# Kernel tuning notes

Measured on AMD Instinct MI355X. Metric: run time of the kernel, lower is better.

The kernel has to match this reference:

```python
import jax, jax.numpy as jnp
import numpy as np

N = 10000      # nodes
E = 320000     # edges (avg degree 32)
H = 128        # hidden_channels
G = 50         # num_gaussians
NF = 128       # num_filters
L = 6          # num_interactions
CUTOFF = 10.0


def ssp(x):
    # ShiftedSoftplus: softplus(x) - log(2)
    return jax.nn.softplus(x) - jnp.log(2.0).astype(x.dtype)


def setup_inputs() -> dict:
    key = jax.random.key(0)
    ks = jax.random.split(key, 16)
    s = 0.05
    return {
        "z": jax.random.normal(ks[0], (N, H), jnp.float32),
        "pos": jax.random.normal(ks[1], (N, 3), jnp.float32) * 3.0,
        "edge_index": jax.random.randint(ks[2], (2, E), 0, N, dtype=jnp.int64),
        # per-layer stacked parameters (PyTorch Linear convention: y = x @ W.T + b)
        "mlp1_w": jax.random.normal(ks[3], (L, NF, G), jnp.float32) * s,
        "mlp1_b": jnp.zeros((L, NF), jnp.float32),
        "mlp2_w": jax.random.normal(ks[4], (L, NF, NF), jnp.float32) * s,
        "mlp2_b": jnp.zeros((L, NF), jnp.float32),
        "lin1_w": jax.random.normal(ks[5], (L, NF, H), jnp.float32) * s,   # no bias
        "lin2_w": jax.random.normal(ks[6], (L, H, NF), jnp.float32) * s,
        "lin2_b": jnp.zeros((L, H), jnp.float32),
        "lin_w": jax.random.normal(ks[7], (L, H, H), jnp.float32) * s,
        "lin_b": jnp.zeros((L, H), jnp.float32),
        "coord_w": jax.random.normal(ks[8], (L, 1, G + 2 * H), jnp.float32) * s,
        "coord_b": jnp.zeros((L, 1), jnp.float32),
    }


def reference(z, pos, edge_index, mlp1_w, mlp1_b, mlp2_w, mlp2_b,
              lin1_w, lin2_w, lin2_b, lin_w, lin_b, coord_w, coord_b):
    row, col = edge_index[0], edge_index[1]
    # edge distances from INITIAL positions (computed once, as in torch code)
    edge_weight = jnp.linalg.norm(pos[row] - pos[col], axis=-1)          # [E]
    offset = jnp.linspace(0.0, CUTOFF, G).astype(pos.dtype)              # [G]
    coeff = -0.5 / (offset[1] - offset[0]) ** 2
    edge_attr = jnp.exp(coeff * (edge_weight[:, None] - offset[None, :]) ** 2)  # [E,G]
    C = 0.5 * (jnp.cos(edge_weight * jnp.pi / CUTOFF) + 1.0)             # [E] cosine cutoff
    ones_e = jnp.ones((E,), pos.dtype)
    h = z
    for l in range(L):
        # ---- coordinate update (uses current pos and current h) ----
        feat = jnp.concatenate([edge_attr, h[row], h[col]], axis=-1)     # [E, G+2H]
        cw = feat @ coord_w[l].T + coord_b[l]                            # [E,1]
        aggr = (pos[row] - pos[col]) * cw                                # [E,3]
        sums = jax.ops.segment_sum(aggr, row, num_segments=N)            # [N,3]
        cnt = jax.ops.segment_sum(ones_e, row, num_segments=N)           # [N]
        mean = jnp.where(cnt[:, None] > 0, sums / jnp.maximum(cnt, 1.0)[:, None], 0.0)
        pos = pos + mean
        # ---- CFConv interaction ----
        Wf = ssp(edge_attr @ mlp1_w[l].T + mlp1_b[l]) @ mlp2_w[l].T + mlp2_b[l]  # [E,NF]
        Wf = Wf * C[:, None]
        xf = h @ lin1_w[l].T                                             # [N,NF]
        agg = jax.ops.segment_sum(xf[row] * Wf, col, num_segments=N)     # [N,NF]
        out = agg @ lin2_w[l].T + lin2_b[l]                              # [N,H]
        h = h + (ssp(out) @ lin_w[l].T + lin_b[l])
    return (pos, h)
```

## Files before the change

### kernel.cpp

```cpp
#include <hip/hip_runtime.h>


#define NN 10000
#define EE 320000
#define HH 128
#define GG 50
#define NF 128
#define NL 6
#define TROWS 2048
#define NB 128

typedef unsigned short u16;
typedef unsigned int u32;
typedef short bf16x8 __attribute__((ext_vector_type(8)));
typedef float f32x4  __attribute__((ext_vector_type(4)));

__device__ __forceinline__ float us2f(u16 u){
  union { float f; u32 i; } v; v.i = ((u32)u) << 16; return v.f;
}
__device__ __forceinline__ u16 f2us(float x){
  union { float f; u32 i; } v; v.f = x;
  u32 r = v.i + 0x7fffu + ((v.i >> 16) & 1u);
  return (u16)(r >> 16);
}
__device__ __forceinline__ float ldin(const void* p, int i, int bf){
  return bf ? us2f(((const u16*)p)[i]) : ((const float*)p)[i];
}
__device__ __forceinline__ float sspf(float x){
  return fmaxf(x, 0.f) + __logf(1.f + __expf(-fabsf(x))) - 0.6931472f;
}
__device__ __forceinline__ int detect_bf(const u32* __restrict__ zraw){
  int lane = threadIdx.x & 63;
  int c = 0;
  #pragma unroll
  for(int j=0;j<4;j++){
    u32 w = zraw[lane*4+j];
    u32 hb = (w >> 8) & 0x7F;
    c += (hb >= 0x38 && hb <= 0x41) ? 1 : 0;
  }
  return __popcll(__ballot(c >= 2)) >= 32;
}
__device__ __forceinline__ int detect_i64(const int* __restrict__ ei_raw){
  int lane = threadIdx.x & 63;
  int c = 0;
  #pragma unroll
  for(int j=0;j<4;j++) c += (ei_raw[2*(lane*4+j)+1] == 0) ? 1 : 0;
  return __popcll(__ballot(c >= 3)) >= 32;
}

__global__ void k_prep(const u32* __restrict__ zraw, const void* __restrict__ pos_in,
    const void* __restrict__ mlp1_w, const void* __restrict__ mlp1_b,
    const void* __restrict__ mlp2_w, const void* __restrict__ mlp2_b,
    const void* __restrict__ lin1_w, const void* __restrict__ lin2_w,
    const void* __restrict__ lin2_b, const void* __restrict__ lin_w,
    const void* __restrict__ lin_b,  const void* __restrict__ coord_w,
    const void* __restrict__ coord_b,
    float* __restrict__ h, float* __restrict__ pc40, int* __restrict__ wmaxi,
    float* __restrict__ b1f, float* __restrict__ b2v,
    u16* __restrict__ w1b, u16* __restrict__ w2bb,
    u16* __restrict__ l1b, u16* __restrict__ l2b,
    float* __restrict__ l2bf, u16* __restrict__ lwb,
    float* __restrict__ lbf, float* __restrict__ cwf, float* __restrict__ cbf)
{
  int bf = detect_bf(zraw);
  int b = blockIdx.x;
  if(b < NN*HH/256){
    int i = b*256 + threadIdx.x;
    h[i] = ldin(zraw, i, bf);
    if(i < NN*3){
      int n = i/3, comp = i%3;
      pc40[n*4 + comp] = ldin(pos_in, i, bf);
    }
    if(i == 0) *wmaxi = 0;
  } else {
    int i = (b - NN*HH/256)*256 + threadIdx.x;
    if(i < NL*NF){
      b1f[i]  = ldin(mlp1_b, i, bf);
      b2v[i]  = ldin(mlp2_b, i, bf);
      l2bf[i] = ldin(lin2_b, i, bf);
      lbf[i]  = ldin(lin_b,  i, bf);
    }
    if(i < NL*NF*64){
      int l = i/(NF*64), rem = i%(NF*64);
      int f = rem>>6, g = rem&63;
      w1b[i] = (g < GG) ? f2us(ldin(mlp1_w, (l*NF + f)*GG + g, bf)) : (u16)0;
    }
    if(i < NL*NF*NF){
      w2bb[i] = f2us(ldin(mlp2_w, i, bf));
      l1b[i]  = f2us(ldin(lin1_w, i, bf));
      l2b[i]  = f2us(ldin(lin2_w, i, bf));
      lwb[i]  = f2us(ldin(lin_w,  i, bf));
    }
    if(i < NL*(GG+2*HH)) cwf[i] = ldin(coord_w, i, bf);
    if(i < NL) cbf[i] = ldin(coord_b, i, bf);
  }
}

__global__ void k_count(const int* __restrict__ ei_raw, const float* __restrict__ pc4,
                        int* __restrict__ eiN, float* __restrict__ wE,
                        u32* __restrict__ partR32, u32* __restrict__ partC32,
                        int* __restrict__ wmaxi){
  __shared__ u32 hr[NN/2];
  __shared__ u32 hc[NN/2];
  int is64 = detect_i64(ei_raw);
  int b = blockIdx.x, tid = threadIdx.x;
  for(int i=tid; i<NN/2; i+=256){ hr[i]=0; hc[i]=0; }
  __syncthreads();
  int e0 = b*(EE/NB), e1 = e0 + EE/NB;
  float wm = 0.f;
  for(int e = e0 + tid; e < e1; e += 256){
    int r = is64 ? ei_raw[2*e] : ei_raw[e];
    int c = is64 ? ei_raw[2*(EE+e)] : ei_raw[EE+e];
    eiN[e] = r; eiN[EE+e] = c;
    float4 pr = *(const float4*)&pc4[r*4];
    float4 pcv = *(const float4*)&pc4[c*4];
    float dx = pr.x-pcv.x, dy = pr.y-pcv.y, dz = pr.z-pcv.z;
    float w = sqrtf(dx*dx + dy*dy + dz*dz);
    wE[e] = w;
    wm = fmaxf(wm, w);
    atomicAdd(&hr[r>>1], (r&1) ? 0x10000u : 1u);
    atomicAdd(&hc[c>>1], (c&1) ? 0x10000u : 1u);
  }
  #pragma unroll
  for(int s=32; s>0; s>>=1) wm = fmaxf(wm, __shfl_down(wm, s, 64));
  if((tid & 63) == 0) atomicMax(wmaxi, __float_as_int(wm));
  __syncthreads();
  for(int i=tid; i<NN/2; i+=256){
    partR32[(size_t)b*(NN/2) + i] = hr[i];
    partC32[(size_t)b*(NN/2) + i] = hc[i];
  }
}

__global__ void k_scan2(const int* __restrict__ col_deg, const int* __restrict__ deg_row,
                        int* __restrict__ col_start, int* __restrict__ row_start){
  __shared__ int pc[1024];
  __shared__ int pr[1024];
  int tid = threadIdx.x;
  const int CH = (NN + 1023)/1024;
  int base = tid*CH;
  int sc = 0, sr = 0;
  for(int i=0;i<CH;i++){
    int idx = base+i;
    if(idx<NN){ sc += col_deg[idx]; sr += deg_row[idx]; }
  }
  pc[tid] = sc; pr[tid] = sr;
  __syncthreads();
  for(int off=1; off<1024; off<<=1){
    int vc = (tid>=off) ? pc[tid-off] : 0;
    int vr = (tid>=off) ? pr[tid-off] : 0;
    __syncthreads();
    pc[tid] += vc; pr[tid] += vr;
    __syncthreads();
  }
  int runc = (tid==0) ? 0 : pc[tid-1];
  int runr = (tid==0) ? 0 : pr[tid-1];
  for(int i=0;i<CH;i++){
    int idx = base+i;
    if(idx<NN){
      col_start[idx]=runc; runc += col_deg[idx];
      row_start[idx]=runr; runr += deg_row[idx];
    }
  }
  if(tid==1023){ col_start[NN] = runc; row_start[NN] = runr; }
}

__global__ void k_fill(const int* __restrict__ eiN, const float* __restrict__ wE,
                       const int* __restrict__ col_start, const int* __restrict__ row_start,
                       const u16* __restrict__ partR16, const u16* __restrict__ partC16,
                       int* __restrict__ row_s, float* __restrict__ wEs,
                       int* __restrict__ rcol_s, float* __restrict__ rw_s){
  __shared__ u32 hr[NN/2];
  __shared__ u32 hc[NN/2];
  int b = blockIdx.x, t = threadIdx.x;
  for(int i=t; i<NN/2; i+=256){ hr[i]=0; hc[i]=0; }
  __syncthreads();
  int e0 = b*(EE/NB), e1 = e0 + EE/NB;
  for(int e = e0 + t; e < e1; e += 256){
    int r = eiN[e], c = eiN[EE+e];
    float w = wE[e];
    u32 oldc = atomicAdd(&hc[c>>1], (c&1) ? 0x10000u : 1u);
    u32 rkc = (c&1) ? (oldc >> 16) : (oldc & 0xFFFFu);
    int p = col_start[c] + (int)partC16[(size_t)b*NN + c] + (int)rkc;
    row_s[p] = r; wEs[p] = w;
    u32 oldr = atomicAdd(&hr[r>>1], (r&1) ? 0x10000u : 1u);
    u32 rkr = (r&1) ? (oldr >> 16) : (oldr & 0xFFFFu);
    int p2 = row_start[r] + (int)partR16[(size_t)b*NN + r] + (int)rkr;
    rcol_s[p2] = c; rw_s[p2] = w;
  }
}

__global__ void k_tabnode(const u16* __restrict__ w1b, const float* __restrict__ b1f,
                          const u16* __restrict__ w2bb, const float* __restrict__ b2v,
                          const float* __restrict__ cwf, const int* __restrict__ wmaxi,
                          u16* __restrict__ tabB, float* __restrict__ tabS,
                          const float* __restrict__ h, const u16* __restrict__ l1b,
                          u16* __restrict__ xfb0, float* __restrict__ dr0,
                          float* __restrict__ pc40,
                          u16* __restrict__ partR16, u16* __restrict__ partC16,
                          int* __restrict__ degR, int* __restrict__ degC){
  __shared__ __align__(16) u16 S[32*72 + 32*136];
  int b = blockIdx.x, t = threadIdx.x;
  int wave = t >> 6, lane = t & 63;
  int m16 = lane & 15, quad = lane >> 4;
  if(b < NL*64){
    int l = b >> 6;
    int r0 = (b & 63)*32;
    u16* attr = S;
    u16* t1   = S + 32*72;
    float delta = __int_as_float(*wmaxi) / (float)(TROWS-1);
    for(int idx=t; idx<32*64; idx+=256){
      int r = idx >> 6, g = idx & 63;
      float w = (float)(r0 + r)*delta;
      float d = w - (float)g*(10.f/49.f);
      attr[r*72 + g] = (g < GG) ? f2us(__expf(-12.005f*d*d)) : (u16)0;
    }
    __syncthreads();
    {
      const u16* __restrict__ w1 = w1b + (size_t)l*NF*64;
      f32x4 acc[2][2];
      #pragma unroll
      for(int nc=0;nc<2;nc++){
        float bv = b1f[l*NF + wave*32 + nc*16 + m16];
        #pragma unroll
        for(int mr=0;mr<2;mr++) acc[mr][nc] = (f32x4){bv,bv,bv,bv};
      }
      #pragma unroll
      for(int ks=0; ks<2; ks++){
        bf16x8 aA[2], bB[2];
        #pragma unroll
        for(int mr=0;mr<2;mr++)
          aA[mr] = *(const bf16x8*)&attr[(mr*16 + m16)*72 + ks*32 + quad*8];
        #pragma unroll
        for(int nc=0;nc<2;nc++)
          bB[nc] = *(const bf16x8*)&w1[(wave*32 + nc*16 + m16)*64 + ks*32 + quad*8];
        #pragma unroll
        for(int mr=0;mr<2;mr++)
          #pragma unroll
          for(int nc=0;nc<2;nc++)
            acc[mr][nc] = __builtin_amdgcn_mfma_f32_16x16x32_bf16(aA[mr], bB[nc], acc[mr][nc], 0,0,0);
      }
      #pragma unroll
      for(int mr=0;mr<2;mr++)
        #pragma unroll
        for(int nc=0;nc<2;nc++)
          #pragma unroll
          for(int r=0;r<4;r++)
            t1[(mr*16 + quad*4 + r)*136 + wave*32 + nc*16 + m16] = f2us(sspf(acc[mr][nc][r]));
    }
    __syncthreads();
    {
      const u16* __restrict__ w2 = w2bb + (size_t)l*NF*NF;
      f32x4 acc[2][2];
      #pragma unroll
      for(int nc=0;nc<2;nc++){
        float bv = b2v[l*NF + wave*32 + nc*16 + m16];
        #pragma unroll
        for(int mr=0;mr<2;mr++) acc[mr][nc] = (f32x4){bv,bv,bv,bv};
      }
      #pragma unroll
      for(int ks=0; ks<4; ks++){
        bf16x8 aA[2], bB[2];
        #pragma unroll
        for(int mr=0;mr<2;mr++)
          aA[mr] = *(const bf16x8*)&t1[(mr*16 + m16)*136 + ks*32 + quad*8];
        #pragma unroll
        for(int nc=0;nc<2;nc++)
          bB[nc] = *(const bf16x8*)&w2[(wave*32 + nc*16 + m16)*NF + ks*32 + quad*8];
        #pragma unroll
        for(int mr=0;mr<2;mr++)
          #pragma unroll
          for(int nc=0;nc<2;nc++)
            acc[mr][nc] = __builtin_amdgcn_mfma_f32_16x16x32_bf16(aA[mr], bB[nc], acc[mr][nc], 0,0,0);
      }
      #pragma unroll
      for(int mr=0;mr<2;mr++){
        #pragma unroll
        for(int r=0;r<4;r++){
          int row = r0 + mr*16 + quad*4 + r;
          float w = (float)row*delta;
          float C = 0.5f*(cosf(w*0.3141592653589793f) + 1.f);
          #pragma unroll
          for(int nc=0;nc<2;nc++)
            tabB[((size_t)l*TROWS + row)*NF + wave*32 + nc*16 + m16] = f2us(acc[mr][nc][r]*C);
        }
      }
    }
    if(t < 32){
      const float* __restrict__ cwg = cwf + l*(GG+2*HH);
      float w = (float)(r0 + t)*delta;
      float s = 0.f;
      for(int g=0; g<GG; g++){
        float d = w - (float)g*(10.f/49.f);
        s += __expf(-12.005f*d*d)*cwg[g];
      }
      tabS[l*TROWS + r0 + t] = s;
    }
  } else if(b < NL*64 + NN/16){
    int n0 = (b - NL*64)*16;
    u16* T = S;
    {
      int node = t >> 4, c0 = (t & 15)*8;
      const float* hp = &h[(n0 + node)*HH + c0];
      f32x4 v0 = *(const f32x4*)hp;
      f32x4 v1 = *(const f32x4*)(hp+4);
      u16* d = &T[node*136 + c0];
      d[0]=f2us(v0[0]); d[1]=f2us(v0[1]); d[2]=f2us(v0[2]); d[3]=f2us(v0[3]);
      d[4]=f2us(v1[0]); d[5]=f2us(v1[1]); d[6]=f2us(v1[2]); d[7]=f2us(v1[3]);
    }
    __syncthreads();
    {
      const float* __restrict__ cw = cwf;
      int j = t >> 4, l16 = t & 15;
      float ar = 0.f, ac = 0.f;
      #pragma unroll
      for(int i=0;i<8;i++){
        float hvv = us2f(T[j*136 + l16 + 16*i]);
        ar += hvv*cw[GG + l16 + 16*i];
        ac += hvv*cw[GG + HH + l16 + 16*i];
      }
      #pragma unroll
      for(int s=8; s>0; s>>=1){
        ar += __shfl_down(ar, s, 16);
        ac += __shfl_down(ac, s, 16);
      }
      if(l16 == 0){ dr0[n0+j] = ar; pc40[(n0+j)*4+3] = ac; }
    }
    {
      const u16* __restrict__ wC = l1b;
      bf16x8 aH[4];
      #pragma unroll
      for(int ks=0; ks<4; ks++)
        aH[ks] = *(const bf16x8*)&T[m16*136 + ks*32 + quad*8];
      #pragma unroll
      for(int nc=0; nc<2; nc++){
        int fcol = wave*32 + nc*16 + m16;
        f32x4 acc = (f32x4){0.f,0.f,0.f,0.f};
        #pragma unroll
        for(int ks=0; ks<4; ks++){
          bf16x8 bbv = *(const bf16x8*)&wC[fcol*HH + ks*32 + quad*8];
          acc = __builtin_amdgcn_mfma_f32_16x16x32_bf16(aH[ks], bbv, acc, 0,0,0);
        }
        #pragma unroll
        for(int r=0;r<4;r++)
          xfb0[(n0+quad*4+r)*NF + fcol] = f2us(acc[r]);
      }
    }
  } else {
    int n = (b - (NL*64 + NN/16))*256 + t;
    if(n >= NN) return;
    u32 rr = 0, rc = 0;
    for(int b0=0; b0<NB; b0+=8){
      u32 vr[8], vc[8];
      #pragma unroll
      for(int j=0;j<8;j++){
        vr[j] = partR16[(size_t)(b0+j)*NN + n];
        vc[j] = partC16[(size_t)(b0+j)*NN + n];
      }
      #pragma unroll
      for(int j=0;j<8;j++){
        partR16[(size_t)(b0+j)*NN + n] = (u16)rr; rr += vr[j];
        partC16[(size_t)(b0+j)*NN + n] = (u16)rc; rc += vc[j];
      }
    }
    degR[n] = (int)rr; degC[n] = (int)rc;
  }
}

__global__ void k_layer(const int* __restrict__ col_start, const int* __restrict__ row_s,
                        const float* __restrict__ wEs, const u32* __restrict__ xfR,
                        u16* __restrict__ xfW,
                        const u16* __restrict__ tabB, const int* __restrict__ wmaxi,
                        int l,
                        const u16* __restrict__ l2b, const float* __restrict__ l2bf,
                        const u16* __restrict__ lwb, const float* __restrict__ lbf,
                        float* __restrict__ h, const u16* __restrict__ l1b,
                        const float* __restrict__ cwf,
                        const float* __restrict__ drR, float* __restrict__ drW,
                        const int* __restrict__ row_start, const int* __restrict__ rcol_s,
                        const float* __restrict__ rw_s, const float* __restrict__ tabS,
                        const float* __restrict__ cbf,
                        const float* __restrict__ pc4R, float* __restrict__ pc4W,
                        const u32* __restrict__ zraw, void* __restrict__ out){
  __shared__ __align__(16) u16 T[16*136];
  __shared__ __align__(16) u16 T2[16*136];
  int b = blockIdx.x, t = threadIdx.x;
  float invD = (float)(TROWS-1) / __int_as_float(*wmaxi);
  int wave = t >> 6, lane = t & 63;

  if(b % 3 == 0){
    int n0 = (b/3)*16;
    {
      const u32* __restrict__ tg32 = (const u32*)(tabB + (size_t)l*TROWS*NF);
      u32* __restrict__ T32 = (u32*)T;
      #pragma unroll
      for(int j=0;j<2;j++){
        int n = n0 + wave*2 + j;
        int p0 = col_start[n], p1 = col_start[n+1];
        float aa[4] = {0.f,0.f,0.f,0.f};
        float bb[4] = {0.f,0.f,0.f,0.f};
        int p = p0;
        for(; p+8 <= p1; p += 8){
          u32 gv[8], xv[8];
          #pragma unroll
          for(int k=0;k<8;k++){
            int r = row_s[p+k];
            int i0 = min((int)(wEs[p+k]*invD + 0.5f), TROWS-1);
            gv[k] = tg32[i0*64 + lane];
            xv[k] = xfR[r*64 + lane];
          }
          #pragma unroll
          for(int k=0;k<8;k++){
            aa[k&3] += us2f((u16)xv[k])      * us2f((u16)gv[k]);
            bb[k&3] += us2f((u16)(xv[k]>>16))* us2f((u16)(gv[k]>>16));
          }
        }
        for(; p < p1; p++){
          int r = row_s[p];
          int i0 = min((int)(wEs[p]*invD + 0.5f), TROWS-1);
          u32 g = tg32[i0*64 + lane];
          u32 x = xfR[r*64 + lane];
          aa[0] += us2f((u16)x)      * us2f((u16)g);
          bb[0] += us2f((u16)(x>>16))* us2f((u16)(g>>16));
        }
        float av = (aa[0]+aa[1])+(aa[2]+aa[3]);
        float bv = (bb[0]+bb[1])+(bb[2]+bb[3]);
        T32[(wave*2+j)*68 + lane] = (u32)f2us(av) | ((u32)f2us(bv) << 16);
      }
    }
    __syncthreads();
    int m16 = lane & 15, quad = lane >> 4;
    int fcol = wave*16 + m16;
    f32x4 acc;
    {
      bf16x8 aA[4];
      #pragma unroll
      for(int ks=0; ks<4; ks++)
        aA[ks] = *(const bf16x8*)&T[m16*136 + ks*32 + quad*8];
      const u16* __restrict__ wA = l2b + l*HH*NF;
      float bv = l2bf[l*HH + fcol];
      acc = (f32x4){bv,bv,bv,bv};
      #pragma unroll
      for(int ks=0; ks<4; ks++){
        bf16x8 bbv = *(const bf16x8*)&wA[fcol*NF + ks*32 + quad*8];
        acc = __builtin_amdgcn_mfma_f32_16x16x32_bf16(aA[ks], bbv, acc, 0,0,0);
      }
      #pragma unroll
      for(int r=0;r<4;r++)
        T2[(quad*4+r)*136 + fcol] = f2us(sspf(acc[r]));
    }
    __syncthreads();
    float hv[4];
    int bf = (l == NL-1) ? detect_bf(zraw) : 0;
    {
      bf16x8 aS[4];
      #pragma unroll
      for(int ks=0; ks<4; ks++)
        aS[ks] = *(const bf16x8*)&T2[m16*136 + ks*32 + quad*8];
      const u16* __restrict__ wB = lwb + l*HH*HH;
      float bv = lbf[l*HH + fcol];
      acc = (f32x4){bv,bv,bv,bv};
      #pragma unroll
      for(int ks=0; ks<4; ks++){
        bf16x8 bbv = *(const bf16x8*)&wB[fcol*HH + ks*32 + quad*8];
        acc = __builtin_amdgcn_mfma_f32_16x16x32_bf16(aS[ks], bbv, acc, 0,0,0);
      }
      #pragma unroll
      for(int r=0;r<4;r++)
        hv[r] = h[(n0+quad*4+r)*HH + fcol] + acc[r];
    }
    if(l == NL-1){
      #pragma unroll
      for(int r=0;r<4;r++){
        int n = n0 + quad*4 + r;
        if(bf) ((u16*)out)[NN*3 + n*HH + fcol] = f2us(hv[r]);
        else   ((float*)out)[NN*3 + n*HH + fcol] = hv[r];
      }
      return;
    }
    #pragma unroll
    for(int r=0;r<4;r++){
      int n = n0 + quad*4 + r;
      h[n*HH + fcol] = hv[r];
      T[(quad*4+r)*136 + fcol] = f2us(hv[r]);
    }
    __syncthreads();
    {
      bf16x8 aH[4];
      #pragma unroll
      for(int ks=0; ks<4; ks++)
        aH[ks] = *(const bf16x8*)&T[m16*136 + ks*32 + quad*8];
      const u16* __restrict__ wC = l1b + (l+1)*NF*HH;
      acc = (f32x4){0.f,0.f,0.f,0.f};
      #pragma unroll
      for(int ks=0; ks<4; ks++){
        bf16x8 bbv = *(const bf16x8*)&wC[fcol*HH + ks*32 + quad*8];
        acc = __builtin_amdgcn_mfma_f32_16x16x32_bf16(aH[ks], bbv, acc, 0,0,0);
      }
      #pragma unroll
      for(int r=0;r<4;r++)
        xfW[(n0+quad*4+r)*NF + fcol] = f2us(acc[r]);
    }
    {
      const float* __restrict__ cw = cwf + (l+1)*(GG + 2*HH);
      int j = t >> 5, l32 = t & 31;
      float ar = 0.f, ac = 0.f;
      #pragma unroll
      for(int i=0;i<4;i++){
        float hvv = us2f(T[j*136 + l32 + 32*i]);
        ar += hvv*cw[GG + l32 + 32*i];
        ac += hvv*cw[GG + HH + l32 + 32*i];
      }
      #pragma unroll
      for(int s=16; s>0; s>>=1){
        ar += __shfl_down(ar, s, 32);
        ac += __shfl_down(ac, s, 32);
      }
      if(l32 == 0){ drW[n0+j] = ar; pc4W[(n0+j)*4+3] = ac; }
    }
  } else {
    int u = b - b/3 - 1;
    int bf = (l == NL-1) ? detect_bf(zraw) : 0;
    int n = u*8 + wave;
    const float* __restrict__ ts = tabS + l*TROWS;
    float cb = cbf[l] + drR[n];
    int p0 = row_start[n], p1 = row_start[n+1];
    float4 pn = *(const float4*)&pc4R[n*4];
    float sx=0.f, sy=0.f, sz=0.f;
    for(int p = p0 + lane; p < p1; p += 64){
      int c = rcol_s[p];
      int i0 = min((int)(rw_s[p]*invD + 0.5f), TROWS-1);
      float4 pcv = *(const float4*)&pc4R[c*4];
      float a = cb + pcv.w + ts[i0];
      sx += (pn.x - pcv.x)*a;
      sy += (pn.y - pcv.y)*a;
      sz += (pn.z - pcv.z)*a;
    }
    #pragma unroll
    for(int s=32; s>0; s>>=1){
      sx += __shfl_down(sx, s, 64);
      sy += __shfl_down(sy, s, 64);
      sz += __shfl_down(sz, s, 64);
    }
    if(lane == 0){
      int cnt = p1 - p0;
      float inv = (cnt > 0) ? 1.f/(float)cnt : 0.f;
      float ox = pn.x + sx*inv, oy = pn.y + sy*inv, oz = pn.z + sz*inv;
      if(l == NL-1){
        if(bf){
          u16* o = (u16*)out;
          o[n*3+0] = f2us(ox); o[n*3+1] = f2us(oy); o[n*3+2] = f2us(oz);
        } else {
          float* o = (float*)out;
          o[n*3+0] = ox; o[n*3+1] = oy; o[n*3+2] = oz;
        }
      } else {
        pc4W[n*4+0] = ox; pc4W[n*4+1] = oy; pc4W[n*4+2] = oz;
      }
    }
  }
}

extern "C" void kernel_launch(void* const* d_in, const int* in_sizes, int n_in,
                              void* d_out, int out_size, void* d_ws, size_t ws_size,
                              hipStream_t stream){
  const u32*  z      = (const u32*)d_in[0];
  const void* pos_in = d_in[1];
  const int*  ei_raw = (const int*)d_in[2];
  const void* mlp1_w = d_in[3];
  const void* mlp1_b = d_in[4];
  const void* mlp2_w = d_in[5];
  const void* mlp2_b = d_in[6];
  const void* lin1_w = d_in[7];
  const void* lin2_w = d_in[8];
  const void* lin2_b = d_in[9];
  const void* lin_w  = d_in[10];
  const void* lin_b  = d_in[11];
  const void* coord_w= d_in[12];
  const void* coord_b= d_in[13];

  float* W = (float*)d_ws;
  float* h    = W; W += NN*HH;
  float* pc40 = W; W += NN*4;
  float* pc41 = W; W += NN*4;
  float* dr0  = W; W += NN;
  float* dr1  = W; W += NN;
  float* wE   = W; W += EE;
  float* wEs  = W; W += EE;
  float* rw_s = W; W += EE;
  float* b1f  = W; W += NL*NF;
  float* b2v  = W; W += NL*NF;
  float* l2bf = W; W += NL*HH;
  float* lbf  = W; W += NL*HH;
  float* cwf  = W; W += NL*(GG+2*HH);
  float* cbf  = W; W += NL;
  W = (float*)(((uintptr_t)W + 63) & ~(uintptr_t)63);
  u16*  tabB = (u16*)W; W += (size_t)NL*TROWS*NF/2;
  float* tabS = W; W += NL*TROWS;
  u16* w1b  = (u16*)W; W += (NL*NF*64)/2;
  u16* w2bb = (u16*)W; W += (NL*NF*NF)/2;
  u16* l1b  = (u16*)W; W += (NL*NF*NF)/2;
  u16* l2b  = (u16*)W; W += (NL*NF*NF)/2;
  u16* lwb  = (u16*)W; W += (NL*NF*NF)/2;
  u16* xfb0 = (u16*)W; W += (NN*NF)/2;
  u16* xfb1 = (u16*)W; W += (NN*NF)/2;
  u16* partR16 = (u16*)W; W += (size_t)NB*NN/2;
  u16* partC16 = (u16*)W; W += (size_t)NB*NN/2;
  int* degR      = (int*)W; W += NN;
  int* degC      = (int*)W; W += NN;
  int* col_start = (int*)W; W += NN+1;
  int* row_start = (int*)W; W += NN+1;
  int* row_s     = (int*)W; W += EE;
  int* rcol_s    = (int*)W; W += EE;
  int* eiN       = (int*)W; W += 2*EE;
  int* wmaxi     = (int*)W; W += 1;

  k_prep<<<NN*HH/256 + NL*NF*NF/256, 256, 0, stream>>>(
      z, pos_in, mlp1_w, mlp1_b, mlp2_w, mlp2_b, lin1_w, lin2_w, lin2_b,
      lin_w, lin_b, coord_w, coord_b,
      h, pc40, wmaxi,
      b1f, b2v, w1b, w2bb, l1b, l2b, l2bf, lwb, lbf, cwf, cbf);
  k_count<<<NB, 256, 0, stream>>>(ei_raw, pc40, eiN, wE,
                                  (u32*)partR16, (u32*)partC16, wmaxi);
  k_tabnode<<<NL*64 + NN/16 + (NN+255)/256, 256, 0, stream>>>(
      w1b, b1f, w2bb, b2v, cwf, wmaxi, tabB, tabS,
      h, l1b, xfb0, dr0, pc40,
      partR16, partC16, degR, degC);
  k_scan2<<<1, 1024, 0, stream>>>(degC, degR, col_start, row_start);
  k_fill<<<NB, 256, 0, stream>>>(eiN, wE, col_start, row_start, partR16, partC16,
                                 row_s, wEs, rcol_s, rw_s);

  for(int l=0; l<NL; l++){
    int par = l & 1;
    const u32* xfR = (const u32*)(par ? xfb1 : xfb0);
    u16* xfW = par ? xfb0 : xfb1;
    const float* drR = par ? dr1 : dr0;   float* drW = par ? dr0 : dr1;
    const float* p4R = par ? pc41 : pc40; float* p4W = par ? pc40 : pc41;
    k_layer<<<3*(NN/16), 512, 0, stream>>>(
        col_start, row_s, wEs, xfR, xfW, tabB, wmaxi, l,
        l2b, l2bf, lwb, lbf, h, l1b, cwf,
        drR, drW,
        row_start, rcol_s, rw_s, tabS, cbf, p4R, p4W, z, d_out);
  }
}
```

Measured before the change: 383.6 us.

## Record per-edge ranks in count pass, parallelize fill, double-buffer gather loads

The count kernel now saves each edge's local rank from its shared-memory atomic into per-edge u16 arrays. This lets the fill kernel become a flat one-thread-per-edge scatter over many blocks instead of 128 blocks that redo the shared histogram atomics. Separately, the per-node gather loop in the layer kernel is software-pipelined with two register buffers, so the next eight loads are issued before the current eight are consumed. The cost is extra global traffic for the rank arrays and higher register pressure in the layer kernel.

```diff
diff --git a/kernel.cpp b/kernel.cpp
--- a/kernel.cpp
+++ b/kernel.cpp
@@ -99,6 +99,7 @@
 __global__ void k_count(const int* __restrict__ ei_raw, const float* __restrict__ pc4,
                         int* __restrict__ eiN, float* __restrict__ wE,
                         u32* __restrict__ partR32, u32* __restrict__ partC32,
+                        u16* __restrict__ rkR16, u16* __restrict__ rkC16,
                         int* __restrict__ wmaxi){
   __shared__ u32 hr[NN/2];
   __shared__ u32 hc[NN/2];
@@ -118,8 +119,10 @@
     float w = sqrtf(dx*dx + dy*dy + dz*dz);
     wE[e] = w;
     wm = fmaxf(wm, w);
-    atomicAdd(&hr[r>>1], (r&1) ? 0x10000u : 1u);
-    atomicAdd(&hc[c>>1], (c&1) ? 0x10000u : 1u);
+    u32 or_ = atomicAdd(&hr[r>>1], (r&1) ? 0x10000u : 1u);
+    rkR16[e] = (u16)((r&1) ? (or_ >> 16) : (or_ & 0xFFFFu));
+    u32 oc_ = atomicAdd(&hc[c>>1], (c&1) ? 0x10000u : 1u);
+    rkC16[e] = (u16)((c&1) ? (oc_ >> 16) : (oc_ & 0xFFFFu));
   }
   #pragma unroll
   for(int s=32; s>0; s>>=1) wm = fmaxf(wm, __shfl_down(wm, s, 64));
@@ -167,26 +170,18 @@
 __global__ void k_fill(const int* __restrict__ eiN, const float* __restrict__ wE,
                        const int* __restrict__ col_start, const int* __restrict__ row_start,
                        const u16* __restrict__ partR16, const u16* __restrict__ partC16,
+                       const u16* __restrict__ rkR16, const u16* __restrict__ rkC16,
                        int* __restrict__ row_s, float* __restrict__ wEs,
                        int* __restrict__ rcol_s, float* __restrict__ rw_s){
-  __shared__ u32 hr[NN/2];
-  __shared__ u32 hc[NN/2];
-  int b = blockIdx.x, t = threadIdx.x;
-  for(int i=t; i<NN/2; i+=256){ hr[i]=0; hc[i]=0; }
-  __syncthreads();
-  int e0 = b*(EE/NB), e1 = e0 + EE/NB;
-  for(int e = e0 + t; e < e1; e += 256){
-    int r = eiN[e], c = eiN[EE+e];
-    float w = wE[e];
-    u32 oldc = atomicAdd(&hc[c>>1], (c&1) ? 0x10000u : 1u);
-    u32 rkc = (c&1) ? (oldc >> 16) : (oldc & 0xFFFFu);
-    int p = col_start[c] + (int)partC16[(size_t)b*NN + c] + (int)rkc;
-    row_s[p] = r; wEs[p] = w;
-    u32 oldr = atomicAdd(&hr[r>>1], (r&1) ? 0x10000u : 1u);
-    u32 rkr = (r&1) ? (oldr >> 16) : (oldr & 0xFFFFu);
-    int p2 = row_start[r] + (int)partR16[(size_t)b*NN + r] + (int)rkr;
-    rcol_s[p2] = c; rw_s[p2] = w;
-  }
+  int e = blockIdx.x*256 + threadIdx.x;
+  if(e >= EE) return;
+  int r = eiN[e], c = eiN[EE+e];
+  float w = wE[e];
+  int b = e / (EE/NB);
+  int p = col_start[c] + (int)partC16[(size_t)b*NN + c] + (int)rkC16[e];
+  row_s[p] = r; wEs[p] = w;
+  int p2 = row_start[r] + (int)partR16[(size_t)b*NN + r] + (int)rkR16[e];
+  rcol_s[p2] = c; rw_s[p2] = w;
 }
 
 __global__ void k_tabnode(const u16* __restrict__ w1b, const float* __restrict__ b1f,
@@ -398,22 +393,43 @@
         int p0 = col_start[n], p1 = col_start[n+1];
         float aa[4] = {0.f,0.f,0.f,0.f};
         float bb[4] = {0.f,0.f,0.f,0.f};
+        u32 gA[8], xA[8], gB[8], xB[8];
+#define LOAD8(G,X,Q) { \
+        _Pragma("unroll") \
+        for(int k=0;k<8;k++){ \
+          int r_ = row_s[(Q)+k]; \
+          int i0_ = min((int)(wEs[(Q)+k]*invD + 0.5f), TROWS-1); \
+          G[k] = tg32[i0_*64 + lane]; \
+          X[k] = xfR[r_*64 + lane]; \
+        } }
+#define CONS8(G,X) { \
+        _Pragma("unroll") \
+        for(int k=0;k<8;k++){ \
+          aa[k&3] += us2f((u16)X[k])      * us2f((u16)G[k]); \
+          bb[k&3] += us2f((u16)(X[k]>>16))* us2f((u16)(G[k]>>16)); \
+        } }
         int p = p0;
-        for(; p+8 <= p1; p += 8){
-          u32 gv[8], xv[8];
-          #pragma unroll
-          for(int k=0;k<8;k++){
-            int r = row_s[p+k];
-            int i0 = min((int)(wEs[p+k]*invD + 0.5f), TROWS-1);
-            gv[k] = tg32[i0*64 + lane];
-            xv[k] = xfR[r*64 + lane];
+        int nb = (p1 - p0) >> 3;
+        if(nb){
+          LOAD8(gA,xA,p);
+          int i = 1;
+          for(; i+1 < nb; i += 2){
+            LOAD8(gB,xB, p + i*8);
+            CONS8(gA,xA);
+            LOAD8(gA,xA, p + i*8 + 8);
+            CONS8(gB,xB);
           }
-          #pragma unroll
-          for(int k=0;k<8;k++){
-            aa[k&3] += us2f((u16)xv[k])      * us2f((u16)gv[k]);
-            bb[k&3] += us2f((u16)(xv[k]>>16))* us2f((u16)(gv[k]>>16));
+          if(i < nb){
+            LOAD8(gB,xB, p + i*8);
+            CONS8(gA,xA);
+            CONS8(gB,xB);
+          } else {
+            CONS8(gA,xA);
           }
+          p += nb*8;
         }
+#undef LOAD8
+#undef CONS8
         for(; p < p1; p++){
           int r = row_s[p];
           int i0 = min((int)(wEs[p]*invD + 0.5f), TROWS-1);
@@ -605,6 +621,8 @@
   u16* xfb1 = (u16*)W; W += (NN*NF)/2;
   u16* partR16 = (u16*)W; W += (size_t)NB*NN/2;
   u16* partC16 = (u16*)W; W += (size_t)NB*NN/2;
+  u16* rkR16 = (u16*)W; W += EE/2;
+  u16* rkC16 = (u16*)W; W += EE/2;
   int* degR      = (int*)W; W += NN;
   int* degC      = (int*)W; W += NN;
   int* col_start = (int*)W; W += NN+1;
@@ -620,14 +638,15 @@
       h, pc40, wmaxi,
       b1f, b2v, w1b, w2bb, l1b, l2b, l2bf, lwb, lbf, cwf, cbf);
   k_count<<<NB, 256, 0, stream>>>(ei_raw, pc40, eiN, wE,
-                                  (u32*)partR16, (u32*)partC16, wmaxi);
+                                  (u32*)partR16, (u32*)partC16, rkR16, rkC16, wmaxi);
   k_tabnode<<<NL*64 + NN/16 + (NN+255)/256, 256, 0, stream>>>(
       w1b, b1f, w2bb, b2v, cwf, wmaxi, tabB, tabS,
       h, l1b, xfb0, dr0, pc40,
       partR16, partC16, degR, degC);
   k_scan2<<<1, 1024, 0, stream>>>(degC, degR, col_start, row_start);
-  k_fill<<<NB, 256, 0, stream>>>(eiN, wE, col_start, row_start, partR16, partC16,
-                                 row_s, wEs, rcol_s, rw_s);
+  k_fill<<<EE/256, 256, 0, stream>>>(eiN, wE, col_start, row_start,
+                                     partR16, partC16, rkR16, rkC16,
+                                     row_s, wEs, rcol_s, rw_s);
 
   for(int l=0; l<NL; l++){
     int par = l & 1;
```

New measurement: 397.7 us. +3.7%, slower.

## Pack sorted edge source and distance bin into one word; rebalance layer blocks

Applied to the files above, without the earlier changes.

The CSR edge arrays now store a single 32-bit word per edge, holding the node index and the precomputed table bin. This replaces a separate int and float plus a per-layer quantisation step, which cuts gather traffic in every layer. The fill kernel no longer recomputes ranks with shared-memory atomics. k_count records per-edge ranks, and k_fill becomes one thread per edge. The layer kernel changes its block split from 1 conv block (16 nodes) per 2 coord blocks to 1 conv block (8 nodes, one wave each) per coord block. The MFMA tiles are now half-empty, with zero padding rows and masked stores.

```diff
diff --git a/kernel.cpp b/kernel.cpp
--- a/kernel.cpp
+++ b/kernel.cpp
@@ -99,6 +99,7 @@
 __global__ void k_count(const int* __restrict__ ei_raw, const float* __restrict__ pc4,
                         int* __restrict__ eiN, float* __restrict__ wE,
                         u32* __restrict__ partR32, u32* __restrict__ partC32,
+                        u16* __restrict__ rkR16, u16* __restrict__ rkC16,
                         int* __restrict__ wmaxi){
   __shared__ u32 hr[NN/2];
   __shared__ u32 hc[NN/2];
@@ -118,8 +119,10 @@
     float w = sqrtf(dx*dx + dy*dy + dz*dz);
     wE[e] = w;
     wm = fmaxf(wm, w);
-    atomicAdd(&hr[r>>1], (r&1) ? 0x10000u : 1u);
-    atomicAdd(&hc[c>>1], (c&1) ? 0x10000u : 1u);
+    u32 or_ = atomicAdd(&hr[r>>1], (r&1) ? 0x10000u : 1u);
+    rkR16[e] = (u16)((r&1) ? (or_ >> 16) : (or_ & 0xFFFFu));
+    u32 oc_ = atomicAdd(&hc[c>>1], (c&1) ? 0x10000u : 1u);
+    rkC16[e] = (u16)((c&1) ? (oc_ >> 16) : (oc_ & 0xFFFFu));
   }
   #pragma unroll
   for(int s=32; s>0; s>>=1) wm = fmaxf(wm, __shfl_down(wm, s, 64));
@@ -167,26 +170,19 @@
 __global__ void k_fill(const int* __restrict__ eiN, const float* __restrict__ wE,
                        const int* __restrict__ col_start, const int* __restrict__ row_start,
                        const u16* __restrict__ partR16, const u16* __restrict__ partC16,
-                       int* __restrict__ row_s, float* __restrict__ wEs,
-                       int* __restrict__ rcol_s, float* __restrict__ rw_s){
-  __shared__ u32 hr[NN/2];
-  __shared__ u32 hc[NN/2];
-  int b = blockIdx.x, t = threadIdx.x;
-  for(int i=t; i<NN/2; i+=256){ hr[i]=0; hc[i]=0; }
-  __syncthreads();
-  int e0 = b*(EE/NB), e1 = e0 + EE/NB;
-  for(int e = e0 + t; e < e1; e += 256){
-    int r = eiN[e], c = eiN[EE+e];
-    float w = wE[e];
-    u32 oldc = atomicAdd(&hc[c>>1], (c&1) ? 0x10000u : 1u);
-    u32 rkc = (c&1) ? (oldc >> 16) : (oldc & 0xFFFFu);
-    int p = col_start[c] + (int)partC16[(size_t)b*NN + c] + (int)rkc;
-    row_s[p] = r; wEs[p] = w;
-    u32 oldr = atomicAdd(&hr[r>>1], (r&1) ? 0x10000u : 1u);
-    u32 rkr = (r&1) ? (oldr >> 16) : (oldr & 0xFFFFu);
-    int p2 = row_start[r] + (int)partR16[(size_t)b*NN + r] + (int)rkr;
-    rcol_s[p2] = c; rw_s[p2] = w;
-  }
+                       const u16* __restrict__ rkR16, const u16* __restrict__ rkC16,
+                       const int* __restrict__ wmaxi,
+                       u32* __restrict__ pk_s, u32* __restrict__ pkr_s){
+  int e = blockIdx.x*256 + threadIdx.x;
+  if(e >= EE) return;
+  int r = eiN[e], c = eiN[EE+e];
+  float invD = (float)(TROWS-1) / __int_as_float(*wmaxi);
+  u32 i0 = (u32)min((int)(wE[e]*invD + 0.5f), TROWS-1);
+  int b = e / (EE/NB);
+  int p = col_start[c] + (int)partC16[(size_t)b*NN + c] + (int)rkC16[e];
+  pk_s[p] = ((u32)r << 11) | i0;
+  int p2 = row_start[r] + (int)partR16[(size_t)b*NN + r] + (int)rkR16[e];
+  pkr_s[p2] = ((u32)c << 11) | i0;
 }
 
 __global__ void k_tabnode(const u16* __restrict__ w1b, const float* __restrict__ b1f,
@@ -366,66 +362,59 @@
   }
 }
 
-__global__ void k_layer(const int* __restrict__ col_start, const int* __restrict__ row_s,
-                        const float* __restrict__ wEs, const u32* __restrict__ xfR,
-                        u16* __restrict__ xfW,
-                        const u16* __restrict__ tabB, const int* __restrict__ wmaxi,
-                        int l,
+__global__ void k_layer(const int* __restrict__ col_start, const u32* __restrict__ pk_s,
+                        const u32* __restrict__ xfR, u16* __restrict__ xfW,
+                        const u16* __restrict__ tabB, int l,
                         const u16* __restrict__ l2b, const float* __restrict__ l2bf,
                         const u16* __restrict__ lwb, const float* __restrict__ lbf,
                         float* __restrict__ h, const u16* __restrict__ l1b,
                         const float* __restrict__ cwf,
                         const float* __restrict__ drR, float* __restrict__ drW,
-                        const int* __restrict__ row_start, const int* __restrict__ rcol_s,
-                        const float* __restrict__ rw_s, const float* __restrict__ tabS,
-                        const float* __restrict__ cbf,
+                        const int* __restrict__ row_start, const u32* __restrict__ pkr_s,
+                        const float* __restrict__ tabS, const float* __restrict__ cbf,
                         const float* __restrict__ pc4R, float* __restrict__ pc4W,
                         const u32* __restrict__ zraw, void* __restrict__ out){
   __shared__ __align__(16) u16 T[16*136];
   __shared__ __align__(16) u16 T2[16*136];
   int b = blockIdx.x, t = threadIdx.x;
-  float invD = (float)(TROWS-1) / __int_as_float(*wmaxi);
   int wave = t >> 6, lane = t & 63;
 
-  if(b % 3 == 0){
-    int n0 = (b/3)*16;
+  if((b & 1) == 0){
+    int n0 = (b >> 1)*8;
     {
       const u32* __restrict__ tg32 = (const u32*)(tabB + (size_t)l*TROWS*NF);
       u32* __restrict__ T32 = (u32*)T;
-      #pragma unroll
-      for(int j=0;j<2;j++){
-        int n = n0 + wave*2 + j;
-        int p0 = col_start[n], p1 = col_start[n+1];
-        float aa[4] = {0.f,0.f,0.f,0.f};
-        float bb[4] = {0.f,0.f,0.f,0.f};
-        int p = p0;
-        for(; p+8 <= p1; p += 8){
-          u32 gv[8], xv[8];
-          #pragma unroll
-          for(int k=0;k<8;k++){
-            int r = row_s[p+k];
-            int i0 = min((int)(wEs[p+k]*invD + 0.5f), TROWS-1);
-            gv[k] = tg32[i0*64 + lane];
-            xv[k] = xfR[r*64 + lane];
-          }
-          #pragma unroll
-          for(int k=0;k<8;k++){
-            aa[k&3] += us2f((u16)xv[k])      * us2f((u16)gv[k]);
-            bb[k&3] += us2f((u16)(xv[k]>>16))* us2f((u16)(gv[k]>>16));
-          }
+      int n = n0 + wave;
+      int p0 = col_start[n], p1 = col_start[n+1];
+      float aa[4] = {0.f,0.f,0.f,0.f};
+      float bb[4] = {0.f,0.f,0.f,0.f};
+      int p = p0;
+      for(; p+8 <= p1; p += 8){
+        u32 pk[8], gv[8], xv[8];
+        #pragma unroll
+        for(int k=0;k<8;k++) pk[k] = pk_s[p+k];
+        #pragma unroll
+        for(int k=0;k<8;k++){
+          gv[k] = tg32[(pk[k] & 2047u)*64 + lane];
+          xv[k] = xfR[(pk[k] >> 11)*64 + lane];
         }
-        for(; p < p1; p++){
-          int r = row_s[p];
-          int i0 = min((int)(wEs[p]*invD + 0.5f), TROWS-1);
-          u32 g = tg32[i0*64 + lane];
-          u32 x = xfR[r*64 + lane];
-          aa[0] += us2f((u16)x)      * us2f((u16)g);
-          bb[0] += us2f((u16)(x>>16))* us2f((u16)(g>>16));
+        #pragma unroll
+        for(int k=0;k<8;k++){
+          aa[k&3] += us2f((u16)xv[k])      * us2f((u16)gv[k]);
+          bb[k&3] += us2f((u16)(xv[k]>>16))* us2f((u16)(gv[k]>>16));
         }
-        float av = (aa[0]+aa[1])+(aa[2]+aa[3]);
-        float bv = (bb[0]+bb[1])+(bb[2]+bb[3]);
-        T32[(wave*2+j)*68 + lane] = (u32)f2us(av) | ((u32)f2us(bv) << 16);
-      }
+      }
+      for(; p < p1; p++){
+        u32 pk = pk_s[p];
+        u32 g = tg32[(pk & 2047u)*64 + lane];
+        u32 x = xfR[(pk >> 11)*64 + lane];
+        aa[0] += us2f((u16)x)      * us2f((u16)g);
+        bb[0] += us2f((u16)(x>>16))* us2f((u16)(g>>16));
+      }
+      float av = (aa[0]+aa[1])+(aa[2]+aa[3]);
+      float bv = (bb[0]+bb[1])+(bb[2]+bb[3]);
+      T32[wave*68 + lane] = (u32)f2us(av) | ((u32)f2us(bv) << 16);
+      T32[(8+wave)*68 + lane] = 0;
     }
     __syncthreads();
     int m16 = lane & 15, quad = lane >> 4;
@@ -464,24 +453,30 @@
         bf16x8 bbv = *(const bf16x8*)&wB[fcol*HH + ks*32 + quad*8];
         acc = __builtin_amdgcn_mfma_f32_16x16x32_bf16(aS[ks], bbv, acc, 0,0,0);
       }
-      #pragma unroll
-      for(int r=0;r<4;r++)
-        hv[r] = h[(n0+quad*4+r)*HH + fcol] + acc[r];
+      if(quad < 2){
+        #pragma unroll
+        for(int r=0;r<4;r++)
+          hv[r] = h[(n0+quad*4+r)*HH + fcol] + acc[r];
+      }
     }
     if(l == NL-1){
+      if(quad < 2){
+        #pragma unroll
+        for(int r=0;r<4;r++){
+          int n = n0 + quad*4 + r;
+          if(bf) ((u16*)out)[NN*3 + n*HH + fcol] = f2us(hv[r]);
+          else   ((float*)out)[NN*3 + n*HH + fcol] = hv[r];
+        }
+      }
+      return;
+    }
+    if(quad < 2){
       #pragma unroll
       for(int r=0;r<4;r++){
         int n = n0 + quad*4 + r;
-        if(bf) ((u16*)out)[NN*3 + n*HH + fcol] = f2us(hv[r]);
-        else   ((float*)out)[NN*3 + n*HH + fcol] = hv[r];
-      }
-      return;
-    }
-    #pragma unroll
-    for(int r=0;r<4;r++){
-      int n = n0 + quad*4 + r;
-      h[n*HH + fcol] = hv[r];
-      T[(quad*4+r)*136 + fcol] = f2us(hv[r]);
+        h[n*HH + fcol] = hv[r];
+        T[(quad*4+r)*136 + fcol] = f2us(hv[r]);
+      }
     }
     __syncthreads();
     {
@@ -496,29 +491,30 @@
         bf16x8 bbv = *(const bf16x8*)&wC[fcol*HH + ks*32 + quad*8];
         acc = __builtin_amdgcn_mfma_f32_16x16x32_bf16(aH[ks], bbv, acc, 0,0,0);
       }
-      #pragma unroll
-      for(int r=0;r<4;r++)
-        xfW[(n0+quad*4+r)*NF + fcol] = f2us(acc[r]);
+      if(quad < 2){
+        #pragma unroll
+        for(int r=0;r<4;r++)
+          xfW[(n0+quad*4+r)*NF + fcol] = f2us(acc[r]);
+      }
     }
     {
       const float* __restrict__ cw = cwf + (l+1)*(GG + 2*HH);
-      int j = t >> 5, l32 = t & 31;
       float ar = 0.f, ac = 0.f;
       #pragma unroll
-      for(int i=0;i<4;i++){
-        float hvv = us2f(T[j*136 + l32 + 32*i]);
-        ar += hvv*cw[GG + l32 + 32*i];
-        ac += hvv*cw[GG + HH + l32 + 32*i];
-      }
-      #pragma unroll
-      for(int s=16; s>0; s>>=1){
-        ar += __shfl_down(ar, s, 32);
-        ac += __shfl_down(ac, s, 32);
-      }
-      if(l32 == 0){ drW[n0+j] = ar; pc4W[(n0+j)*4+3] = ac; }
+      for(int i=0;i<2;i++){
+        float hvv = us2f(T[wave*136 + lane + 64*i]);
+        ar += hvv*cw[GG + lane + 64*i];
+        ac += hvv*cw[GG + HH + lane + 64*i];
+      }
+      #pragma unroll
+      for(int s=32; s>0; s>>=1){
+        ar += __shfl_down(ar, s, 64);
+        ac += __shfl_down(ac, s, 64);
+      }
+      if(lane == 0){ drW[n0+wave] = ar; pc4W[(n0+wave)*4+3] = ac; }
     }
   } else {
-    int u = b - b/3 - 1;
+    int u = b >> 1;
     int bf = (l == NL-1) ? detect_bf(zraw) : 0;
     int n = u*8 + wave;
     const float* __restrict__ ts = tabS + l*TROWS;
@@ -527,10 +523,10 @@
     float4 pn = *(const float4*)&pc4R[n*4];
     float sx=0.f, sy=0.f, sz=0.f;
     for(int p = p0 + lane; p < p1; p += 64){
-      int c = rcol_s[p];
-      int i0 = min((int)(rw_s[p]*invD + 0.5f), TROWS-1);
+      u32 pk = pkr_s[p];
+      int c = (int)(pk >> 11);
       float4 pcv = *(const float4*)&pc4R[c*4];
-      float a = cb + pcv.w + ts[i0];
+      float a = cb + pcv.w + ts[pk & 2047u];
       sx += (pn.x - pcv.x)*a;
       sy += (pn.y - pcv.y)*a;
       sz += (pn.z - pcv.z)*a;
@@ -585,8 +581,6 @@
   float* dr0  = W; W += NN;
   float* dr1  = W; W += NN;
   float* wE   = W; W += EE;
-  float* wEs  = W; W += EE;
-  float* rw_s = W; W += EE;
   float* b1f  = W; W += NL*NF;
   float* b2v  = W; W += NL*NF;
   float* l2bf = W; W += NL*HH;
@@ -605,12 +599,14 @@
   u16* xfb1 = (u16*)W; W += (NN*NF)/2;
   u16* partR16 = (u16*)W; W += (size_t)NB*NN/2;
   u16* partC16 = (u16*)W; W += (size_t)NB*NN/2;
+  u16* rkR16 = (u16*)W; W += EE/2;
+  u16* rkC16 = (u16*)W; W += EE/2;
   int* degR      = (int*)W; W += NN;
   int* degC      = (int*)W; W += NN;
   int* col_start = (int*)W; W += NN+1;
   int* row_start = (int*)W; W += NN+1;
-  int* row_s     = (int*)W; W += EE;
-  int* rcol_s    = (int*)W; W += EE;
+  u32* pk_s      = (u32*)W; W += EE;
+  u32* pkr_s     = (u32*)W; W += EE;
   int* eiN       = (int*)W; W += 2*EE;
   int* wmaxi     = (int*)W; W += 1;
 
@@ -620,14 +616,15 @@
       h, pc40, wmaxi,
       b1f, b2v, w1b, w2bb, l1b, l2b, l2bf, lwb, lbf, cwf, cbf);
   k_count<<<NB, 256, 0, stream>>>(ei_raw, pc40, eiN, wE,
-                                  (u32*)partR16, (u32*)partC16, wmaxi);
+                                  (u32*)partR16, (u32*)partC16, rkR16, rkC16, wmaxi);
   k_tabnode<<<NL*64 + NN/16 + (NN+255)/256, 256, 0, stream>>>(
       w1b, b1f, w2bb, b2v, cwf, wmaxi, tabB, tabS,
       h, l1b, xfb0, dr0, pc40,
       partR16, partC16, degR, degC);
   k_scan2<<<1, 1024, 0, stream>>>(degC, degR, col_start, row_start);
-  k_fill<<<NB, 256, 0, stream>>>(eiN, wE, col_start, row_start, partR16, partC16,
-                                 row_s, wEs, rcol_s, rw_s);
+  k_fill<<<EE/256, 256, 0, stream>>>(eiN, wE, col_start, row_start,
+                                     partR16, partC16, rkR16, rkC16, wmaxi,
+                                     pk_s, pkr_s);
 
   for(int l=0; l<NL; l++){
     int par = l & 1;
@@ -635,10 +632,10 @@
     u16* xfW = par ? xfb0 : xfb1;
     const float* drR = par ? dr1 : dr0;   float* drW = par ? dr0 : dr1;
     const float* p4R = par ? pc41 : pc40; float* p4W = par ? pc40 : pc41;
-    k_layer<<<3*(NN/16), 512, 0, stream>>>(
-        col_start, row_s, wEs, xfR, xfW, tabB, wmaxi, l,
+    k_layer<<<2*(NN/8), 512, 0, stream>>>(
+        col_start, pk_s, xfR, xfW, tabB, l,
         l2b, l2bf, lwb, lbf, h, l1b, cwf,
         drR, drW,
-        row_start, rcol_s, rw_s, tabS, cbf, p4R, p4W, z, d_out);
-  }
-}
+        row_start, pkr_s, tabS, cbf, p4R, p4W, z, d_out);
+  }
+}
```

Result: slower. 466.3 us (+21.5%).
